# Kernel tuning notes

Measured on AMD Instinct MI355X. Metric: run time of the kernel, lower is better.

Reference implementation:

```python
import jax, jax.numpy as jnp
import numpy as np

B, MAXN, D, H, S = 64, 512, 512, 8, 32
DH = D // H          # per-head dim = 64
N = B * MAXN         # 32768 total nodes
E = 524288           # ~avg degree 16
EPS = 1e-5


def setup_inputs() -> dict:
    key = jax.random.key(0)
    ks = jax.random.split(key, 18)
    s = 0.05
    x_dense = jax.random.normal(ks[0], (B, MAXN, D), jnp.float32)
    x = jax.random.normal(ks[1], (N, D), jnp.float32)
    src = jax.random.randint(ks[2], (E,), 0, N)
    # destinations kept within the same graph as the source
    dst = (src // MAXN) * MAXN + jax.random.randint(ks[3], (E,), 0, MAXN)
    edge_index = jnp.stack([src, dst]).astype(jnp.int32)
    batch = (jnp.arange(N) // MAXN).astype(jnp.int32)  # sorted, 512 nodes/graph
    seed = jax.random.normal(ks[4], (S, 1, D), jnp.float32) * s
    # per-head GCN conv weights concatenated along output dim: [D, H*DH] == [D, D]
    Wk = jax.random.normal(ks[5], (D, D), jnp.float32) * s
    bk = jnp.zeros((D,), jnp.float32)
    Wv = jax.random.normal(ks[6], (D, D), jnp.float32) * s
    bv = jnp.zeros((D,), jnp.float32)
    q_proj_weight = jax.random.normal(ks[7], (D, D), jnp.float32) * s
    Wo = jax.random.normal(ks[8], (D, D), jnp.float32) * s
    bo = jnp.zeros((D,), jnp.float32)
    Wff = jax.random.normal(ks[9], (D, D), jnp.float32) * s
    bff = jnp.zeros((D,), jnp.float32)
    gamma_h = jnp.ones((D,), jnp.float32)
    beta_h = jnp.zeros((D,), jnp.float32)
    gamma_z = jnp.ones((D,), jnp.float32)
    beta_z = jnp.zeros((D,), jnp.float32)
    return dict(x_dense=x_dense, x=x, edge_index=edge_index, batch=batch,
                seed=seed, Wk=Wk, bk=bk, Wv=Wv, bv=bv,
                q_proj_weight=q_proj_weight, Wo=Wo, bo=bo, Wff=Wff, bff=bff,
                gamma_h=gamma_h, beta_h=beta_h, gamma_z=gamma_z, beta_z=beta_z)


def _gcn(x, W, b, src, dst):
    # PyG GCNConv with self-loops + symmetric norm; all H heads fused via W [D, H*DH]
    xw = x @ W                                   # [N, D]
    idx = jnp.arange(N)
    src_f = jnp.concatenate([src, idx])
    dst_f = jnp.concatenate([dst, idx])
    deg = jax.ops.segment_sum(jnp.ones_like(dst_f, dtype=x.dtype), dst_f, num_segments=N)
    dinv = jax.lax.rsqrt(deg)                    # deg >= 1 (self-loops)
    norm = dinv[src_f] * dinv[dst_f]             # [E+N]
    out = jax.ops.segment_sum(xw[src_f] * norm[:, None], dst_f, num_segments=N)
    return out + b


def _to_dense(feat, batch):
    # to_dense_batch for sorted batch vector; padded slots are zeros
    counts = jax.ops.segment_sum(jnp.ones((N,), jnp.int32), batch, num_segments=B)
    start = jnp.cumsum(counts) - counts
    pos = jnp.arange(N) - start[batch]
    return jnp.zeros((B, MAXN, feat.shape[-1]), feat.dtype).at[batch, pos].set(feat)


def _layernorm(x, g, b):
    m = jnp.mean(x, -1, keepdims=True)
    v = jnp.mean(jnp.square(x - m), -1, keepdims=True)
    return (x - m) * jax.lax.rsqrt(v + EPS) * g + b


def reference(x_dense, x, edge_index, batch, seed, Wk, bk, Wv, bv,
              q_proj_weight, Wo, bo, Wff, bff, gamma_h, beta_h, gamma_z, beta_z):
    src, dst = edge_index[0], edge_index[1]
    k_nodes = _gcn(x, Wk, bk, src, dst)          # [N, D] (H heads concat)
    v_nodes = _gcn(x, Wv, bv, src, dst)
    k_dense = _to_dense(k_nodes, batch)          # [B, MAXN, D]
    v_dense = _to_dense(v_nodes, batch)

    # query: seed [S,1,D] repeated over batch -> [S,B,D]; q projection (F.linear)
    query = jnp.broadcast_to(seed, (S, B, D))
    q = jnp.einsum('sbd,ed->sbe', query, q_proj_weight)
    scale = 1.0 / jnp.sqrt(jnp.float32(DH))
    qh = (q * scale).reshape(S, B, H, DH).transpose(1, 2, 0, 3)     # [B,H,S,DH]
    kh = k_dense.reshape(B, MAXN, H, DH).transpose(0, 2, 1, 3)      # [B,H,N,DH]
    vh = v_dense.reshape(B, MAXN, H, DH).transpose(0, 2, 1, 3)
    scores = jnp.einsum('bhsd,bhnd->bhsn', qh, kh)                  # [B,H,S,MAXN]
    attn = jax.nn.softmax(scores, axis=-1)                          # no padding mask (faithful)
    ctx = jnp.einsum('bhsn,bhnd->bhsd', attn, vh)                   # [B,H,S,DH]
    ctx = ctx.transpose(0, 2, 1, 3).reshape(B, S, D)                # heads concat
    attn_out = ctx @ Wo.T + bo                                      # [B,S,D]

    query_bse = jnp.broadcast_to(seed.transpose(1, 0, 2), (B, S, D))
    embed = _layernorm(query_bse + attn_out, gamma_h, beta_h)
    embed = _layernorm(embed + embed @ Wff.T + bff, gamma_z, beta_z)
    return embed
```

## Files before the change

### kernel.cpp

```cpp
#include <hip/hip_runtime.h>
#include <hip/hip_bf16.h>

#define BN   64
#define MAXN 512
#define DIM  512
#define NH   8
#define NS   32
#define NN   32768
#define NE   524288
#define MP   (2048 * 512)

typedef __hip_bfloat16 bf16;
using bf16x8 = __attribute__((ext_vector_type(8))) short;
using f32x4  = __attribute__((ext_vector_type(4))) float;

__device__ int   g_cnt[NN];
__device__ int   g_cur[NN];
__device__ int   g_off[NN + 1];
__device__ int   g_csr[NE];
__device__ float g_dinv[NN];
__device__ bf16  g_xb[NN * DIM];
__device__ bf16  g_agg[NN * DIM];
__device__ bf16  g_aggT[NN * DIM];
__device__ bf16  g_qf[256 * DIM];
__device__ bf16  g_wob[DIM * DIM];
__device__ bf16  g_wvb[DIM * DIM];
__device__ bf16  g_wvo[DIM * 8 * DIM];
__device__ float g_bvo[DIM];
__device__ bf16  g_wffT[DIM * DIM];
__device__ float g_q[NS * DIM];
__device__ bf16  g_sc[BN * 256 * MAXN];
__device__ bf16  g_cp[BN * NS * 8 * DIM];
__device__ float g_part[8 * MP];
__device__ float g_h1[BN * NS * DIM];
__device__ bf16  g_h1b[BN * NS * DIM];

__device__ inline float bf2f(unsigned short u) {
    union { unsigned int i; float f; } x; x.i = ((unsigned int)u) << 16; return x.f;
}

__device__ inline void gll16(const bf16* g, bf16* l) {
    __builtin_amdgcn_global_load_lds(
        (const __attribute__((address_space(1))) void*)g,
        (__attribute__((address_space(3))) void*)l, 16, 0, 0);
}

__global__ void k_zero() {
    int i = blockIdx.x * 256 + threadIdx.x;
    if (i < NN) { g_cnt[i] = 0; g_cur[i] = 0; }
}

__global__ void k_count(const int* __restrict__ dst) {
    int e = blockIdx.x * 256 + threadIdx.x;
    if (e < NE) atomicAdd(&g_cnt[dst[e]], 1);
}

__global__ void k_scan() {
    __shared__ int part[1024];
    int t = threadIdx.x;
    int base = t * 32;
    int loc[32]; int s = 0;
#pragma unroll
    for (int i = 0; i < 32; i++) { loc[i] = g_cnt[base + i]; s += loc[i]; }
    part[t] = s; __syncthreads();
    for (int o = 1; o < 1024; o <<= 1) {
        int v = (t >= o) ? part[t - o] : 0;
        __syncthreads();
        part[t] += v;
        __syncthreads();
    }
    int ex = (t == 0) ? 0 : part[t - 1];
#pragma unroll
    for (int i = 0; i < 32; i++) {
        g_off[base + i] = ex; ex += loc[i];
        g_dinv[base + i] = rsqrtf(1.0f + (float)loc[i]);
    }
    if (t == 1023) g_off[NN] = ex;
}

__global__ void k_fill(const int* __restrict__ src, const int* __restrict__ dst) {
    int e = blockIdx.x * 256 + threadIdx.x;
    if (e < NE) {
        int d = dst[e];
        int p = atomicAdd(&g_cur[d], 1);
        g_csr[g_off[d] + p] = src[e];
    }
}

__global__ __launch_bounds__(256) void k_xb(const float* __restrict__ x) {
    long i = (long)(blockIdx.x * 256 + threadIdx.x) * 8;
    int node = (int)(i >> 9);
    float w = g_dinv[node];
    float4 a = *(const float4*)(x + i);
    float4 b = *(const float4*)(x + i + 4);
    float v[8] = {a.x, a.y, a.z, a.w, b.x, b.y, b.z, b.w};
    bf16x8 o;
#pragma unroll
    for (int j = 0; j < 8; j++) { bf16 t = __float2bfloat16(v[j] * w); o[j] = *(short*)&t; }
    *(bf16x8*)(g_xb + i) = o;
}

__global__ __launch_bounds__(256) void k_gather() {
    int bid = blockIdx.x;
    int lb = (bid & 7) * 1024 + (bid >> 3);
    int wave = threadIdx.x >> 6, lane = threadIdx.x & 63;
    int node = lb * 4 + wave;

    bf16x8 sv = ((const bf16x8*)(g_xb + (long)node * DIM))[lane];
    float acc[8];
#pragma unroll
    for (int j = 0; j < 8; j++) acc[j] = bf2f((unsigned short)sv[j]);

    int e = g_off[node], e1 = g_off[node + 1];
    for (; e + 4 <= e1; e += 4) {
        int s0 = g_csr[e], s1 = g_csr[e + 1], s2 = g_csr[e + 2], s3 = g_csr[e + 3];
        bf16x8 r0 = ((const bf16x8*)(g_xb + (long)s0 * DIM))[lane];
        bf16x8 r1 = ((const bf16x8*)(g_xb + (long)s1 * DIM))[lane];
        bf16x8 r2 = ((const bf16x8*)(g_xb + (long)s2 * DIM))[lane];
        bf16x8 r3 = ((const bf16x8*)(g_xb + (long)s3 * DIM))[lane];
#pragma unroll
        for (int j = 0; j < 8; j++)
            acc[j] += (bf2f((unsigned short)r0[j]) + bf2f((unsigned short)r1[j]))
                    + (bf2f((unsigned short)r2[j]) + bf2f((unsigned short)r3[j]));
    }
    for (; e < e1; e++) {
        int s0 = g_csr[e];
        bf16x8 r0 = ((const bf16x8*)(g_xb + (long)s0 * DIM))[lane];
#pragma unroll
        for (int j = 0; j < 8; j++) acc[j] += bf2f((unsigned short)r0[j]);
    }
    float dd = g_dinv[node];
    bf16x8 o;
#pragma unroll
    for (int j = 0; j < 8; j++) { bf16 t = __float2bfloat16(acc[j] * dd); o[j] = *(short*)&t; }
    ((bf16x8*)(g_agg + (long)node * DIM))[lane] = o;
}

__global__ __launch_bounds__(256) void k_aggT() {
    __shared__ unsigned short L[64][72];
    int id = blockIdx.x;
    int b = id >> 6, t = id & 63;
    int n0 = (t & 7) * 64, d0 = (t >> 3) * 64;
    int tid = threadIdx.x;
    const unsigned short* src = (const unsigned short*)g_agg + ((long)b * 512 + n0) * 512 + d0;
#pragma unroll
    for (int p = 0; p < 2; p++) {
        int r = (tid >> 3) + 32 * p, c = (tid & 7) * 8;
        *(int4*)&L[r][c] = *(const int4*)(src + (long)r * 512 + c);
    }
    __syncthreads();
    unsigned short* dst = (unsigned short*)g_aggT + ((long)b * 512 + d0) * 512 + n0;
#pragma unroll
    for (int p = 0; p < 2; p++) {
        int dr = (tid >> 3) + 32 * p, c0 = (tid & 7) * 8;
        unsigned short tmp[8];
#pragma unroll
        for (int j = 0; j < 8; j++) tmp[j] = L[c0 + j][dr];
        *(int4*)(dst + (long)dr * 512 + c0) = *(int4*)tmp;
    }
}

__global__ void k_qproj(const float* __restrict__ seed, const float* __restrict__ Wq) {
    int i = blockIdx.x * 256 + threadIdx.x;
    int s = i >> 9, e = i & 511;
    const float* sr = seed + s * DIM;
    const float* wr = Wq + e * DIM;
    float a0 = 0.f, a1 = 0.f;
    for (int d = 0; d < DIM; d += 8) {
        float4 a = *(const float4*)(sr + d);
        float4 b = *(const float4*)(wr + d);
        float4 c = *(const float4*)(sr + d + 4);
        float4 w = *(const float4*)(wr + d + 4);
        a0 += a.x * b.x + a.y * b.y + a.z * b.z + a.w * b.w;
        a1 += c.x * w.x + c.y * w.y + c.z * w.z + c.w * w.w;
    }
    g_q[i] = (a0 + a1) * 0.125f;
}

__global__ __launch_bounds__(256) void k_cvt(const float* __restrict__ Wo,
                                             const float* __restrict__ Wv,
                                             const float* __restrict__ Wff) {
    long t = blockIdx.x * 256 + threadIdx.x;
    const float* src; bf16* dst; long off;
    if (t < 32768)      { src = Wo;  dst = g_wob;  off = t; }
    else if (t < 65536) { src = Wv;  dst = g_wvb;  off = t - 32768; }
    else                { src = Wff; dst = g_wffT; off = t - 65536; }
    long i = off * 8;
    float4 a = *(const float4*)(src + i);
    float4 b = *(const float4*)(src + i + 4);
    float v[8] = {a.x, a.y, a.z, a.w, b.x, b.y, b.z, b.w};
    bf16x8 o;
#pragma unroll
    for (int j = 0; j < 8; j++) { bf16 q = __float2bfloat16(v[j]); o[j] = *(short*)&q; }
    *(bf16x8*)(dst + i) = o;
}

__global__ __launch_bounds__(256) void k_qf(const float* __restrict__ Wk) {
    int i = blockIdx.x * 256 + threadIdx.x;
    int hs = i >> 9, d = i & 511;
    int h = hs >> 5, s = hs & 31;
    const float* qr = g_q + s * DIM + h * 64;
    const float* wr = Wk + d * DIM + h * 64;
    float a0 = 0.f, a1 = 0.f;
    for (int t2 = 0; t2 < 64; t2 += 8) {
        float4 a = *(const float4*)(qr + t2);
        float4 w = *(const float4*)(wr + t2);
        float4 c = *(const float4*)(qr + t2 + 4);
        float4 u = *(const float4*)(wr + t2 + 4);
        a0 += a.x * w.x + a.y * w.y + a.z * w.z + a.w * w.w;
        a1 += c.x * u.x + c.y * u.y + c.z * u.z + c.w * u.w;
    }
    g_qf[i] = __float2bfloat16(a0 + a1);
}

__global__ __launch_bounds__(256) void k_bvo(const float* __restrict__ bo,
                                             const float* __restrict__ bv,
                                             const float* __restrict__ Wo) {
    int e = blockIdx.x * 256 + threadIdx.x;
    const float* orow = Wo + (long)e * DIM;
    float a0 = 0.f, a1 = 0.f;
    for (int c = 0; c < DIM; c += 8) {
        float4 a = *(const float4*)(bv + c);
        float4 w = *(const float4*)(orow + c);
        float4 x = *(const float4*)(bv + c + 4);
        float4 u = *(const float4*)(orow + c + 4);
        a0 += a.x * w.x + a.y * w.y + a.z * w.z + a.w * w.w;
        a1 += x.x * u.x + x.y * u.y + x.z * u.z + x.w * u.w;
    }
    g_bvo[e] = bo[e] + a0 + a1;
}

__device__ __forceinline__ void gemm128(const bf16* __restrict__ A, long lda,
                                        const bf16* __restrict__ Bt, long ldb,
                                        long row0, long col0, int kbeg, int kend,
                                        bf16 (*As)[128 * 32], bf16 (*Bs)[128 * 32],
                                        f32x4 acc[4][4]) {
    int tid = threadIdx.x;
    int lane = tid & 63, wave = tid >> 6;
    int wr = wave >> 1, wc = wave & 1;
    int fr = lane & 15, fq = lane >> 4;
    int rchunk = (fq ^ ((fr >> 1) & 3)) * 8;
    int u0 = wave * 128 + lane;
    int sr0 = u0 >> 2, sc0 = ((u0 & 3) ^ ((sr0 >> 1) & 3)) * 8;
    int u1 = u0 + 64;
    int sr1 = u1 >> 2, sc1 = ((u1 & 3) ^ ((sr1 >> 1) & 3)) * 8;

    auto stage = [&](int buf, int kt) {
        gll16(A + (row0 + sr0) * lda + kt + sc0, As[buf] + u0 * 8);
        gll16(A + (row0 + sr1) * lda + kt + sc1, As[buf] + u1 * 8);
        gll16(Bt + (col0 + sr0) * ldb + kt + sc0, Bs[buf] + u0 * 8);
        gll16(Bt + (col0 + sr1) * ldb + kt + sc1, Bs[buf] + u1 * 8);
    };

    stage(0, kbeg);
    __syncthreads();
    for (int kt = kbeg; kt < kend; kt += 32) {
        int buf = ((kt - kbeg) >> 5) & 1;
        if (kt + 32 < kend) stage(buf ^ 1, kt + 32);
        bf16x8 af[4], bfv[4];
#pragma unroll
        for (int mi = 0; mi < 4; mi++)
            af[mi] = *(const bf16x8*)(As[buf] + (wr * 64 + mi * 16 + fr) * 32 + rchunk);
#pragma unroll
        for (int ni = 0; ni < 4; ni++)
            bfv[ni] = *(const bf16x8*)(Bs[buf] + (wc * 64 + ni * 16 + fr) * 32 + rchunk);
#pragma unroll
        for (int mi = 0; mi < 4; mi++)
#pragma unroll
            for (int ni = 0; ni < 4; ni++)
                acc[mi][ni] = __builtin_amdgcn_mfma_f32_16x16x32_bf16(af[mi], bfv[ni], acc[mi][ni], 0, 0, 0);
        __syncthreads();
    }
}

#define GEMM_PROLOGUE                                        \
    __shared__ bf16 As[2][128 * 32];                         \
    __shared__ bf16 Bs[2][128 * 32];                         \
    f32x4 acc[4][4];                                         \
    _Pragma("unroll")                                        \
    for (int i = 0; i < 4; i++)                              \
        _Pragma("unroll")                                    \
        for (int j = 0; j < 4; j++) acc[i][j] = (f32x4){0.f, 0.f, 0.f, 0.f}; \
    int lane = threadIdx.x & 63, wave = threadIdx.x >> 6;    \
    int wr = wave >> 1, wc = wave & 1;                       \
    int fr = lane & 15, fq = lane >> 4;

__global__ __launch_bounds__(256) void k_wvo() {
    GEMM_PROLOGUE
    int h = blockIdx.z;
    long row0 = (long)blockIdx.x * 128, col0 = (long)blockIdx.y * 128;
    gemm128(g_wob, DIM, g_wvb, DIM, row0, col0, h * 64, h * 64 + 64, As, Bs, acc);
#pragma unroll
    for (int mi = 0; mi < 4; mi++)
#pragma unroll
        for (int ni = 0; ni < 4; ni++) {
            long col = col0 + wc * 64 + ni * 16 + fr;
#pragma unroll
            for (int r = 0; r < 4; r++) {
                long row = row0 + wr * 64 + mi * 16 + fq * 4 + r;
                g_wvo[row * 4096 + h * 512 + col] = __float2bfloat16(acc[mi][ni][r]);
            }
        }
}

__global__ __launch_bounds__(256) void k_scores() {
    GEMM_PROLOGUE
    int b = blockIdx.z;
    long row0 = (long)blockIdx.x * 128, col0 = (long)blockIdx.y * 128;
    gemm128(g_qf, DIM, g_agg + (long)b * (MAXN * DIM), DIM, row0, col0, 0, DIM, As, Bs, acc);
    bf16* out = g_sc + (long)b * (256 * MAXN);
#pragma unroll
    for (int mi = 0; mi < 4; mi++)
#pragma unroll
        for (int ni = 0; ni < 4; ni++) {
            long col = col0 + wc * 64 + ni * 16 + fr;
#pragma unroll
            for (int r = 0; r < 4; r++) {
                long row = row0 + wr * 64 + mi * 16 + fq * 4 + r;
                out[row * MAXN + col] = __float2bfloat16(acc[mi][ni][r]);
            }
        }
}

__global__ __launch_bounds__(256) void k_soft() {
    int w = threadIdx.x >> 6, lane = threadIdx.x & 63;
    unsigned short* base = (unsigned short*)g_sc + ((long)blockIdx.x * 16 + w * 4) * MAXN;
#pragma unroll
    for (int r = 0; r < 4; r++) {
        unsigned short* row = base + (long)r * MAXN;
        float v[8]; float m = -1e30f;
#pragma unroll
        for (int k = 0; k < 8; k++) { v[k] = bf2f(row[lane + 64 * k]); m = fmaxf(m, v[k]); }
#pragma unroll
        for (int o = 32; o > 0; o >>= 1) m = fmaxf(m, __shfl_xor(m, o));
        float sum = 0.f;
#pragma unroll
        for (int k = 0; k < 8; k++) { v[k] = __expf(v[k] - m); sum += v[k]; }
#pragma unroll
        for (int o = 32; o > 0; o >>= 1) sum += __shfl_xor(sum, o);
        float inv = 1.0f / sum;
#pragma unroll
        for (int k = 0; k < 8; k++) {
            bf16 t = __float2bfloat16(v[k] * inv);
            row[lane + 64 * k] = *(unsigned short*)&t;
        }
    }
}

__global__ __launch_bounds__(256) void k_pvg() {
    GEMM_PROLOGUE
    int z = blockIdx.z, b = z >> 1, dh = z & 1;
    long row0 = (long)blockIdx.x * 128, col0 = (long)blockIdx.y * 128;
    gemm128(g_sc + (long)b * (256 * MAXN), MAXN,
            g_aggT + (long)b * (DIM * MAXN) + (long)dh * (256 * MAXN), MAXN,
            row0, col0, 0, MAXN, As, Bs, acc);
#pragma unroll
    for (int mi = 0; mi < 4; mi++)
#pragma unroll
        for (int ni = 0; ni < 4; ni++) {
            long col = col0 + wc * 64 + ni * 16 + fr;
#pragma unroll
            for (int r = 0; r < 4; r++) {
                long row = row0 + wr * 64 + mi * 16 + fq * 4 + r;
                g_cp[((long)b * NS + (row & 31)) * 4096 + (row >> 5) * 512 + dh * 256 + col] =
                    __float2bfloat16(acc[mi][ni][r]);
            }
        }
}

__global__ __launch_bounds__(256) void k_vo() {
    GEMM_PROLOGUE
    int z = blockIdx.z;
    long row0 = (long)blockIdx.x * 128, col0 = (long)blockIdx.y * 128;
    gemm128(g_cp, 4096, g_wvo, 4096, row0, col0, z * 512, z * 512 + 512, As, Bs, acc);
    float* out = g_part + (long)z * MP;
#pragma unroll
    for (int mi = 0; mi < 4; mi++)
#pragma unroll
        for (int ni = 0; ni < 4; ni++) {
            long col = col0 + wc * 64 + ni * 16 + fr;
#pragma unroll
            for (int r = 0; r < 4; r++) {
                long row = row0 + wr * 64 + mi * 16 + fq * 4 + r;
                out[row * DIM + col] = acc[mi][ni][r];
            }
        }
}

__global__ __launch_bounds__(256) void k_ffn() {
    GEMM_PROLOGUE
    int z = blockIdx.z;
    long row0 = (long)blockIdx.x * 128, col0 = (long)blockIdx.y * 128;
    gemm128(g_h1b, DIM, g_wffT, DIM, row0, col0, z * 128, z * 128 + 128, As, Bs, acc);
    float* out = g_part + (long)z * MP;
#pragma unroll
    for (int mi = 0; mi < 4; mi++)
#pragma unroll
        for (int ni = 0; ni < 4; ni++) {
            long col = col0 + wc * 64 + ni * 16 + fr;
#pragma unroll
            for (int r = 0; r < 4; r++) {
                long row = row0 + wr * 64 + mi * 16 + fq * 4 + r;
                out[row * DIM + col] = acc[mi][ni][r];
            }
        }
}

__device__ inline float blockReduceSum(float v, float* red, int tid) {
#pragma unroll
    for (int o = 32; o > 0; o >>= 1) v += __shfl_xor(v, o);
    __syncthreads();
    if ((tid & 63) == 0) red[tid >> 6] = v;
    __syncthreads();
    return red[0] + red[1] + red[2] + red[3];
}

__global__ __launch_bounds__(256) void k_ln1(const float* __restrict__ seed,
                                             const float* __restrict__ gamma,
                                             const float* __restrict__ beta) {
    __shared__ float red[4];
    int r = blockIdx.x, t = threadIdx.x;
    int s = r & 31;
    long base = (long)r * DIM;
    float v0 = seed[s * DIM + t] + g_bvo[t];
    float v1 = seed[s * DIM + 256 + t] + g_bvo[256 + t];
#pragma unroll
    for (int z = 0; z < 8; z++) {
        v0 += g_part[(long)z * MP + base + t];
        v1 += g_part[(long)z * MP + base + 256 + t];
    }
    float mean = blockReduceSum(v0 + v1, red, t) * (1.0f / DIM);
    float d0 = v0 - mean, d1 = v1 - mean;
    float var = blockReduceSum(d0 * d0 + d1 * d1, red, t) * (1.0f / DIM);
    float ri = rsqrtf(var + 1e-5f);
    float o0 = d0 * ri * gamma[t] + beta[t];
    float o1 = d1 * ri * gamma[256 + t] + beta[256 + t];
    g_h1[base + t] = o0; g_h1[base + 256 + t] = o1;
    g_h1b[base + t] = __float2bfloat16(o0);
    g_h1b[base + 256 + t] = __float2bfloat16(o1);
}

__global__ __launch_bounds__(256) void k_ln2(const float* __restrict__ gamma,
                                             const float* __restrict__ beta,
                                             const float* __restrict__ bff,
                                             float* __restrict__ out) {
    __shared__ float red[4];
    int r = blockIdx.x, t = threadIdx.x;
    long base = (long)r * DIM;
    float v0 = g_h1[base + t] + bff[t];
    float v1 = g_h1[base + 256 + t] + bff[256 + t];
#pragma unroll
    for (int z = 0; z < 4; z++) {
        v0 += g_part[(long)z * MP + base + t];
        v1 += g_part[(long)z * MP + base + 256 + t];
    }
    float mean = blockReduceSum(v0 + v1, red, t) * (1.0f / DIM);
    float d0 = v0 - mean, d1 = v1 - mean;
    float var = blockReduceSum(d0 * d0 + d1 * d1, red, t) * (1.0f / DIM);
    float ri = rsqrtf(var + 1e-5f);
    out[base + t] = d0 * ri * gamma[t] + beta[t];
    out[base + 256 + t] = d1 * ri * gamma[256 + t] + beta[256 + t];
}

extern "C" void kernel_launch(void* const* d_in, const int* in_sizes, int n_in,
                              void* d_out, int out_size, void* d_ws, size_t ws_size,
                              hipStream_t stream) {
    (void)in_sizes; (void)n_in; (void)out_size; (void)d_ws; (void)ws_size;
    const float* x    = (const float*)d_in[1];
    const int*   ei   = (const int*)d_in[2];
    const int*   esrc = ei;
    const int*   edst = ei + NE;
    const float* seed = (const float*)d_in[4];
    const float* Wk   = (const float*)d_in[5];
    const float* Wv   = (const float*)d_in[7];
    const float* bv   = (const float*)d_in[8];
    const float* Wq   = (const float*)d_in[9];
    const float* Wo   = (const float*)d_in[10];
    const float* bo   = (const float*)d_in[11];
    const float* Wff  = (const float*)d_in[12];
    const float* bff  = (const float*)d_in[13];
    const float* gh   = (const float*)d_in[14];
    const float* bh   = (const float*)d_in[15];
    const float* gz   = (const float*)d_in[16];
    const float* bz   = (const float*)d_in[17];
    float* out = (float*)d_out;

    k_zero <<<NN / 256, 256, 0, stream>>>();
    k_count<<<NE / 256, 256, 0, stream>>>(edst);
    k_scan <<<1, 1024, 0, stream>>>();
    k_fill <<<NE / 256, 256, 0, stream>>>(esrc, edst);
    k_xb   <<<(NN * DIM) / (256 * 8), 256, 0, stream>>>(x);
    k_gather<<<NN / 4, 256, 0, stream>>>();
    k_aggT <<<BN * 64, 256, 0, stream>>>();
    k_qproj<<<(NS * DIM) / 256, 256, 0, stream>>>(seed, Wq);
    k_cvt  <<<384, 256, 0, stream>>>(Wo, Wv, Wff);
    k_qf   <<<512, 256, 0, stream>>>(Wk);
    k_wvo  <<<dim3(4, 4, 8), 256, 0, stream>>>();
    k_bvo  <<<2, 256, 0, stream>>>(bo, bv, Wo);

    k_scores<<<dim3(2, 4, BN), 256, 0, stream>>>();
    k_soft  <<<1024, 256, 0, stream>>>();
    k_pvg   <<<dim3(2, 2, BN * 2), 256, 0, stream>>>();

    k_vo <<<dim3(16, 4, 8), 256, 0, stream>>>();
    k_ln1<<<BN * NS, 256, 0, stream>>>(seed, gh, bh);
    k_ffn<<<dim3(16, 4, 4), 256, 0, stream>>>();
    k_ln2<<<BN * NS, 256, 0, stream>>>(gz, bz, bff, out);
}
```

Baseline: 270.5 us.

## Fuse scores, softmax and PV into one attention kernel; merge prep kernels

Replaces the separate scores GEMM, softmax and PV GEMM with a single per-(graph, head) kernel. It computes scores into registers, does the softmax in-block, stores the probabilities in shared memory and multiplies by the transposed aggregate, so the bf16 score buffer round-trip through global memory goes away. The small prep kernels (q projection, weight conversion, qf, Wvo and bias folding) are merged into two launches to cut launch overhead. The Vo split-K drops from 8 to 4, which halves the partial-sum traffic read by the first layernorm. The fused kernel uses a large amount of shared memory and only 512 blocks, so occupancy may be low.

```diff
diff --git a/kernel.cpp b/kernel.cpp
--- a/kernel.cpp
+++ b/kernel.cpp
@@ -29,9 +29,8 @@
 __device__ float g_bvo[DIM];
 __device__ bf16  g_wffT[DIM * DIM];
 __device__ float g_q[NS * DIM];
-__device__ bf16  g_sc[BN * 256 * MAXN];
 __device__ bf16  g_cp[BN * NS * 8 * DIM];
-__device__ float g_part[8 * MP];
+__device__ float g_part[4 * MP];
 __device__ float g_h1[BN * NS * DIM];
 __device__ bf16  g_h1b[BN * NS * DIM];
 
@@ -160,74 +159,57 @@
     }
 }
 
-__global__ void k_qproj(const float* __restrict__ seed, const float* __restrict__ Wq) {
-    int i = blockIdx.x * 256 + threadIdx.x;
-    int s = i >> 9, e = i & 511;
-    const float* sr = seed + s * DIM;
-    const float* wr = Wq + e * DIM;
-    float a0 = 0.f, a1 = 0.f;
-    for (int d = 0; d < DIM; d += 8) {
-        float4 a = *(const float4*)(sr + d);
-        float4 b = *(const float4*)(wr + d);
-        float4 c = *(const float4*)(sr + d + 4);
-        float4 w = *(const float4*)(wr + d + 4);
-        a0 += a.x * b.x + a.y * b.y + a.z * b.z + a.w * b.w;
-        a1 += c.x * w.x + c.y * w.y + c.z * w.z + c.w * w.w;
-    }
-    g_q[i] = (a0 + a1) * 0.125f;
-}
-
-__global__ __launch_bounds__(256) void k_cvt(const float* __restrict__ Wo,
-                                             const float* __restrict__ Wv,
-                                             const float* __restrict__ Wff) {
-    long t = blockIdx.x * 256 + threadIdx.x;
-    const float* src; bf16* dst; long off;
-    if (t < 32768)      { src = Wo;  dst = g_wob;  off = t; }
-    else if (t < 65536) { src = Wv;  dst = g_wvb;  off = t - 32768; }
-    else                { src = Wff; dst = g_wffT; off = t - 65536; }
-    long i = off * 8;
-    float4 a = *(const float4*)(src + i);
-    float4 b = *(const float4*)(src + i + 4);
-    float v[8] = {a.x, a.y, a.z, a.w, b.x, b.y, b.z, b.w};
-    bf16x8 o;
-#pragma unroll
-    for (int j = 0; j < 8; j++) { bf16 q = __float2bfloat16(v[j]); o[j] = *(short*)&q; }
-    *(bf16x8*)(dst + i) = o;
-}
-
-__global__ __launch_bounds__(256) void k_qf(const float* __restrict__ Wk) {
-    int i = blockIdx.x * 256 + threadIdx.x;
-    int hs = i >> 9, d = i & 511;
-    int h = hs >> 5, s = hs & 31;
-    const float* qr = g_q + s * DIM + h * 64;
-    const float* wr = Wk + d * DIM + h * 64;
-    float a0 = 0.f, a1 = 0.f;
-    for (int t2 = 0; t2 < 64; t2 += 8) {
-        float4 a = *(const float4*)(qr + t2);
-        float4 w = *(const float4*)(wr + t2);
-        float4 c = *(const float4*)(qr + t2 + 4);
-        float4 u = *(const float4*)(wr + t2 + 4);
-        a0 += a.x * w.x + a.y * w.y + a.z * w.z + a.w * w.w;
-        a1 += c.x * u.x + c.y * u.y + c.z * u.z + c.w * u.w;
-    }
-    g_qf[i] = __float2bfloat16(a0 + a1);
-}
-
-__global__ __launch_bounds__(256) void k_bvo(const float* __restrict__ bo,
-                                             const float* __restrict__ bv,
-                                             const float* __restrict__ Wo) {
-    int e = blockIdx.x * 256 + threadIdx.x;
-    const float* orow = Wo + (long)e * DIM;
-    float a0 = 0.f, a1 = 0.f;
-    for (int c = 0; c < DIM; c += 8) {
-        float4 a = *(const float4*)(bv + c);
-        float4 w = *(const float4*)(orow + c);
-        float4 x = *(const float4*)(bv + c + 4);
-        float4 u = *(const float4*)(orow + c + 4);
-        a0 += a.x * w.x + a.y * w.y + a.z * w.z + a.w * w.w;
-        a1 += x.x * u.x + x.y * u.y + x.z * u.z + x.w * u.w;
-    }
-    g_bvo[e] = bo[e] + a0 + a1;
+__global__ __launch_bounds__(256) void k_prep(const float* __restrict__ seed,
+                                              const float* __restrict__ Wq,
+                                              const float* __restrict__ Wo,
+                                              const float* __restrict__ Wv,
+                                              const float* __restrict__ Wff,
+                                              const float* __restrict__ bo,
+                                              const float* __restrict__ bv) {
+    int blk = blockIdx.x;
+    if (blk < 64) {
+        int i = blk * 256 + threadIdx.x;
+        int s = i >> 9, e = i & 511;
+        const float* sr = seed + s * DIM;
+        const float* wr = Wq + e * DIM;
+        float a0 = 0.f, a1 = 0.f;
+        for (int d = 0; d < DIM; d += 8) {
+            float4 a = *(const float4*)(sr + d);
+            float4 b = *(const float4*)(wr + d);
+            float4 c = *(const float4*)(sr + d + 4);
+            float4 w = *(const float4*)(wr + d + 4);
+            a0 += a.x * b.x + a.y * b.y + a.z * b.z + a.w * b.w;
+            a1 += c.x * w.x + c.y * w.y + c.z * w.z + c.w * w.w;
+        }
+        g_q[i] = (a0 + a1) * 0.125f;
+    } else if (blk < 448) {
+        long t = (long)(blk - 64) * 256 + threadIdx.x;
+        const float* src; bf16* dst; long off;
+        if (t < 32768)      { src = Wo;  dst = g_wob;  off = t; }
+        else if (t < 65536) { src = Wv;  dst = g_wvb;  off = t - 32768; }
+        else                { src = Wff; dst = g_wffT; off = t - 65536; }
+        long i = off * 8;
+        float4 a = *(const float4*)(src + i);
+        float4 b = *(const float4*)(src + i + 4);
+        float v[8] = {a.x, a.y, a.z, a.w, b.x, b.y, b.z, b.w};
+        bf16x8 o;
+#pragma unroll
+        for (int j = 0; j < 8; j++) { bf16 q = __float2bfloat16(v[j]); o[j] = *(short*)&q; }
+        *(bf16x8*)(dst + i) = o;
+    } else {
+        int e = (blk - 448) * 256 + threadIdx.x;
+        const float* orow = Wo + (long)e * DIM;
+        float a0 = 0.f, a1 = 0.f;
+        for (int c = 0; c < DIM; c += 8) {
+            float4 a = *(const float4*)(bv + c);
+            float4 w = *(const float4*)(orow + c);
+            float4 x = *(const float4*)(bv + c + 4);
+            float4 u = *(const float4*)(orow + c + 4);
+            a0 += a.x * w.x + a.y * w.y + a.z * w.z + a.w * w.w;
+            a1 += x.x * u.x + x.y * u.y + x.z * u.z + x.w * u.w;
+        }
+        g_bvo[e] = bo[e] + a0 + a1;
+    }
 }
 
 __device__ __forceinline__ void gemm128(const bf16* __restrict__ A, long lda,
@@ -273,6 +255,202 @@
     }
 }
 
+__global__ __launch_bounds__(256) void k_qfwvo(const float* __restrict__ Wk) {
+    __shared__ bf16 As[2][128 * 32];
+    __shared__ bf16 Bs[2][128 * 32];
+    int blk = blockIdx.x;
+    if (blk < 512) {
+        int i = blk * 256 + threadIdx.x;
+        int hs = i >> 9, d = i & 511;
+        int h = hs >> 5, s = hs & 31;
+        const float* qr = g_q + s * DIM + h * 64;
+        const float* wr = Wk + d * DIM + h * 64;
+        float a0 = 0.f, a1 = 0.f;
+        for (int t2 = 0; t2 < 64; t2 += 8) {
+            float4 a = *(const float4*)(qr + t2);
+            float4 w = *(const float4*)(wr + t2);
+            float4 c = *(const float4*)(qr + t2 + 4);
+            float4 u = *(const float4*)(wr + t2 + 4);
+            a0 += a.x * w.x + a.y * w.y + a.z * w.z + a.w * w.w;
+            a1 += c.x * u.x + c.y * u.y + c.z * u.z + c.w * u.w;
+        }
+        g_qf[i] = __float2bfloat16(a0 + a1);
+    } else {
+        int wi = blk - 512;
+        int bx = wi & 3, by = (wi >> 2) & 3, h = wi >> 4;
+        f32x4 acc[4][4];
+#pragma unroll
+        for (int i = 0; i < 4; i++)
+#pragma unroll
+            for (int j = 0; j < 4; j++) acc[i][j] = (f32x4){0.f, 0.f, 0.f, 0.f};
+        int lane = threadIdx.x & 63;
+        int wr = (threadIdx.x >> 6) >> 1, wc = (threadIdx.x >> 6) & 1;
+        int fr = lane & 15, fq = lane >> 4;
+        long row0 = (long)bx * 128, col0 = (long)by * 128;
+        gemm128(g_wob, DIM, g_wvb, DIM, row0, col0, h * 64, h * 64 + 64, As, Bs, acc);
+#pragma unroll
+        for (int mi = 0; mi < 4; mi++)
+#pragma unroll
+            for (int ni = 0; ni < 4; ni++) {
+                long col = col0 + wc * 64 + ni * 16 + fr;
+#pragma unroll
+                for (int r = 0; r < 4; r++) {
+                    long row = row0 + wr * 64 + mi * 16 + fq * 4 + r;
+                    g_wvo[row * 4096 + h * 512 + col] = __float2bfloat16(acc[mi][ni][r]);
+                }
+            }
+    }
+}
+
+__global__ __launch_bounds__(256) void k_attn2() {
+    __shared__ bf16 Bs[2][512 * 32];
+    __shared__ bf16 Asq[2][32 * 32];
+    __shared__ bf16 P[32 * 512];
+    __shared__ float redm[4][32];
+    __shared__ float reds[4][32];
+    int z = blockIdx.x;
+    int b = z & 63, h = z >> 6;
+    int tid = threadIdx.x, lane = tid & 63, w = tid >> 6;
+    int fr = lane & 15, fq = lane >> 4;
+    int rchunk = (fq ^ ((fr >> 1) & 3)) * 8;
+
+    const bf16* Aq = g_qf + (long)(h * 32) * DIM;
+    const bf16* Bn = g_agg + (long)b * ((long)MAXN * DIM);
+    const bf16* Bd = g_aggT + (long)b * ((long)DIM * MAXN);
+
+    int brow[8], bcol[8];
+#pragma unroll
+    for (int c = 0; c < 8; c++) {
+        int u = tid + 256 * c;
+        brow[c] = u >> 2;
+        bcol[c] = ((u & 3) ^ ((brow[c] >> 1) & 3)) * 8;
+    }
+    int arow = tid >> 2;
+    int acol = ((tid & 3) ^ ((arow >> 1) & 3)) * 8;
+
+    f32x4 acc[2][8];
+#pragma unroll
+    for (int i = 0; i < 2; i++)
+#pragma unroll
+        for (int j = 0; j < 8; j++) acc[i][j] = (f32x4){0.f, 0.f, 0.f, 0.f};
+
+    if (tid < 128) gll16(Aq + (long)arow * DIM + acol, Asq[0] + tid * 8);
+#pragma unroll
+    for (int c = 0; c < 8; c++)
+        gll16(Bn + (long)brow[c] * DIM + bcol[c], Bs[0] + (tid + 256 * c) * 8);
+    __syncthreads();
+    for (int kt = 0; kt < 512; kt += 32) {
+        int buf = (kt >> 5) & 1;
+        if (kt + 32 < 512) {
+            if (tid < 128) gll16(Aq + (long)arow * DIM + kt + 32 + acol, Asq[buf ^ 1] + tid * 8);
+#pragma unroll
+            for (int c = 0; c < 8; c++)
+                gll16(Bn + (long)brow[c] * DIM + kt + 32 + bcol[c], Bs[buf ^ 1] + (tid + 256 * c) * 8);
+        } else {
+#pragma unroll
+            for (int c = 0; c < 8; c++)
+                gll16(Bd + (long)brow[c] * MAXN + bcol[c], Bs[0] + (tid + 256 * c) * 8);
+        }
+        bf16x8 af[2], bv8[8];
+#pragma unroll
+        for (int mi = 0; mi < 2; mi++)
+            af[mi] = *(const bf16x8*)(Asq[buf] + (mi * 16 + fr) * 32 + rchunk);
+#pragma unroll
+        for (int nf = 0; nf < 8; nf++)
+            bv8[nf] = *(const bf16x8*)(Bs[buf] + (w * 128 + nf * 16 + fr) * 32 + rchunk);
+#pragma unroll
+        for (int mi = 0; mi < 2; mi++)
+#pragma unroll
+            for (int nf = 0; nf < 8; nf++)
+                acc[mi][nf] = __builtin_amdgcn_mfma_f32_16x16x32_bf16(af[mi], bv8[nf], acc[mi][nf], 0, 0, 0);
+        __syncthreads();
+    }
+
+#pragma unroll
+    for (int mi = 0; mi < 2; mi++)
+#pragma unroll
+        for (int r = 0; r < 4; r++) {
+            float m = acc[mi][0][r];
+#pragma unroll
+            for (int nf = 1; nf < 8; nf++) m = fmaxf(m, acc[mi][nf][r]);
+#pragma unroll
+            for (int o = 1; o < 16; o <<= 1) m = fmaxf(m, __shfl_xor(m, o));
+            if (fr == 0) redm[w][mi * 16 + fq * 4 + r] = m;
+        }
+    __syncthreads();
+#pragma unroll
+    for (int mi = 0; mi < 2; mi++)
+#pragma unroll
+        for (int r = 0; r < 4; r++) {
+            int row = mi * 16 + fq * 4 + r;
+            float M = fmaxf(fmaxf(redm[0][row], redm[1][row]), fmaxf(redm[2][row], redm[3][row]));
+            float s = 0.f;
+#pragma unroll
+            for (int nf = 0; nf < 8; nf++) {
+                float e = __expf(acc[mi][nf][r] - M);
+                acc[mi][nf][r] = e; s += e;
+            }
+#pragma unroll
+            for (int o = 1; o < 16; o <<= 1) s += __shfl_xor(s, o);
+            if (fr == 0) reds[w][row] = s;
+        }
+    __syncthreads();
+#pragma unroll
+    for (int mi = 0; mi < 2; mi++)
+#pragma unroll
+        for (int r = 0; r < 4; r++) {
+            int row = mi * 16 + fq * 4 + r;
+            float iv = 1.0f / (reds[0][row] + reds[1][row] + reds[2][row] + reds[3][row]);
+#pragma unroll
+            for (int nf = 0; nf < 8; nf++) {
+                int col = w * 128 + nf * 16 + fr;
+                int ch = (col >> 3) ^ (row & 7);
+                P[row * 512 + ch * 8 + (col & 7)] = __float2bfloat16(acc[mi][nf][r] * iv);
+            }
+        }
+    __syncthreads();
+
+#pragma unroll
+    for (int i = 0; i < 2; i++)
+#pragma unroll
+        for (int j = 0; j < 8; j++) acc[i][j] = (f32x4){0.f, 0.f, 0.f, 0.f};
+    for (int kt = 0; kt < 512; kt += 32) {
+        int buf = (kt >> 5) & 1;
+        if (kt + 32 < 512) {
+#pragma unroll
+            for (int c = 0; c < 8; c++)
+                gll16(Bd + (long)brow[c] * MAXN + kt + 32 + bcol[c], Bs[buf ^ 1] + (tid + 256 * c) * 8);
+        }
+        bf16x8 af2[2], bv8[8];
+#pragma unroll
+        for (int mi = 0; mi < 2; mi++) {
+            int row = mi * 16 + fr;
+            int ch = ((kt >> 3) + fq) ^ (row & 7);
+            af2[mi] = *(const bf16x8*)(P + row * 512 + ch * 8);
+        }
+#pragma unroll
+        for (int nf = 0; nf < 8; nf++)
+            bv8[nf] = *(const bf16x8*)(Bs[buf] + (w * 128 + nf * 16 + fr) * 32 + rchunk);
+#pragma unroll
+        for (int mi = 0; mi < 2; mi++)
+#pragma unroll
+            for (int nf = 0; nf < 8; nf++)
+                acc[mi][nf] = __builtin_amdgcn_mfma_f32_16x16x32_bf16(af2[mi], bv8[nf], acc[mi][nf], 0, 0, 0);
+        __syncthreads();
+    }
+#pragma unroll
+    for (int mi = 0; mi < 2; mi++)
+#pragma unroll
+        for (int nf = 0; nf < 8; nf++) {
+            int d = w * 128 + nf * 16 + fr;
+#pragma unroll
+            for (int r = 0; r < 4; r++) {
+                int s = mi * 16 + fq * 4 + r;
+                g_cp[((long)b * NS + s) * 4096 + h * 512 + d] = __float2bfloat16(acc[mi][nf][r]);
+            }
+        }
+}
+
 #define GEMM_PROLOGUE                                        \
     __shared__ bf16 As[2][128 * 32];                         \
     __shared__ bf16 Bs[2][128 * 32];                         \
@@ -285,94 +463,11 @@
     int wr = wave >> 1, wc = wave & 1;                       \
     int fr = lane & 15, fq = lane >> 4;
 
-__global__ __launch_bounds__(256) void k_wvo() {
-    GEMM_PROLOGUE
-    int h = blockIdx.z;
-    long row0 = (long)blockIdx.x * 128, col0 = (long)blockIdx.y * 128;
-    gemm128(g_wob, DIM, g_wvb, DIM, row0, col0, h * 64, h * 64 + 64, As, Bs, acc);
-#pragma unroll
-    for (int mi = 0; mi < 4; mi++)
-#pragma unroll
-        for (int ni = 0; ni < 4; ni++) {
-            long col = col0 + wc * 64 + ni * 16 + fr;
-#pragma unroll
-            for (int r = 0; r < 4; r++) {
-                long row = row0 + wr * 64 + mi * 16 + fq * 4 + r;
-                g_wvo[row * 4096 + h * 512 + col] = __float2bfloat16(acc[mi][ni][r]);
-            }
-        }
-}
-
-__global__ __launch_bounds__(256) void k_scores() {
-    GEMM_PROLOGUE
-    int b = blockIdx.z;
-    long row0 = (long)blockIdx.x * 128, col0 = (long)blockIdx.y * 128;
-    gemm128(g_qf, DIM, g_agg + (long)b * (MAXN * DIM), DIM, row0, col0, 0, DIM, As, Bs, acc);
-    bf16* out = g_sc + (long)b * (256 * MAXN);
-#pragma unroll
-    for (int mi = 0; mi < 4; mi++)
-#pragma unroll
-        for (int ni = 0; ni < 4; ni++) {
-            long col = col0 + wc * 64 + ni * 16 + fr;
-#pragma unroll
-            for (int r = 0; r < 4; r++) {
-                long row = row0 + wr * 64 + mi * 16 + fq * 4 + r;
-                out[row * MAXN + col] = __float2bfloat16(acc[mi][ni][r]);
-            }
-        }
-}
-
-__global__ __launch_bounds__(256) void k_soft() {
-    int w = threadIdx.x >> 6, lane = threadIdx.x & 63;
-    unsigned short* base = (unsigned short*)g_sc + ((long)blockIdx.x * 16 + w * 4) * MAXN;
-#pragma unroll
-    for (int r = 0; r < 4; r++) {
-        unsigned short* row = base + (long)r * MAXN;
-        float v[8]; float m = -1e30f;
-#pragma unroll
-        for (int k = 0; k < 8; k++) { v[k] = bf2f(row[lane + 64 * k]); m = fmaxf(m, v[k]); }
-#pragma unroll
-        for (int o = 32; o > 0; o >>= 1) m = fmaxf(m, __shfl_xor(m, o));
-        float sum = 0.f;
-#pragma unroll
-        for (int k = 0; k < 8; k++) { v[k] = __expf(v[k] - m); sum += v[k]; }
-#pragma unroll
-        for (int o = 32; o > 0; o >>= 1) sum += __shfl_xor(sum, o);
-        float inv = 1.0f / sum;
-#pragma unroll
-        for (int k = 0; k < 8; k++) {
-            bf16 t = __float2bfloat16(v[k] * inv);
-            row[lane + 64 * k] = *(unsigned short*)&t;
-        }
-    }
-}
-
-__global__ __launch_bounds__(256) void k_pvg() {
-    GEMM_PROLOGUE
-    int z = blockIdx.z, b = z >> 1, dh = z & 1;
-    long row0 = (long)blockIdx.x * 128, col0 = (long)blockIdx.y * 128;
-    gemm128(g_sc + (long)b * (256 * MAXN), MAXN,
-            g_aggT + (long)b * (DIM * MAXN) + (long)dh * (256 * MAXN), MAXN,
-            row0, col0, 0, MAXN, As, Bs, acc);
-#pragma unroll
-    for (int mi = 0; mi < 4; mi++)
-#pragma unroll
-        for (int ni = 0; ni < 4; ni++) {
-            long col = col0 + wc * 64 + ni * 16 + fr;
-#pragma unroll
-            for (int r = 0; r < 4; r++) {
-                long row = row0 + wr * 64 + mi * 16 + fq * 4 + r;
-                g_cp[((long)b * NS + (row & 31)) * 4096 + (row >> 5) * 512 + dh * 256 + col] =
-                    __float2bfloat16(acc[mi][ni][r]);
-            }
-        }
-}
-
 __global__ __launch_bounds__(256) void k_vo() {
     GEMM_PROLOGUE
     int z = blockIdx.z;
     long row0 = (long)blockIdx.x * 128, col0 = (long)blockIdx.y * 128;
-    gemm128(g_cp, 4096, g_wvo, 4096, row0, col0, z * 512, z * 512 + 512, As, Bs, acc);
+    gemm128(g_cp, 4096, g_wvo, 4096, row0, col0, z * 1024, z * 1024 + 1024, As, Bs, acc);
     float* out = g_part + (long)z * MP;
 #pragma unroll
     for (int mi = 0; mi < 4; mi++)
@@ -425,7 +520,7 @@
     float v0 = seed[s * DIM + t] + g_bvo[t];
     float v1 = seed[s * DIM + 256 + t] + g_bvo[256 + t];
 #pragma unroll
-    for (int z = 0; z < 8; z++) {
+    for (int z = 0; z < 4; z++) {
         v0 += g_part[(long)z * MP + base + t];
         v1 += g_part[(long)z * MP + base + 256 + t];
     }
@@ -492,17 +587,12 @@
     k_xb   <<<(NN * DIM) / (256 * 8), 256, 0, stream>>>(x);
     k_gather<<<NN / 4, 256, 0, stream>>>();
     k_aggT <<<BN * 64, 256, 0, stream>>>();
-    k_qproj<<<(NS * DIM) / 256, 256, 0, stream>>>(seed, Wq);
-    k_cvt  <<<384, 256, 0, stream>>>(Wo, Wv, Wff);
-    k_qf   <<<512, 256, 0, stream>>>(Wk);
-    k_wvo  <<<dim3(4, 4, 8), 256, 0, stream>>>();
-    k_bvo  <<<2, 256, 0, stream>>>(bo, bv, Wo);
-
-    k_scores<<<dim3(2, 4, BN), 256, 0, stream>>>();
-    k_soft  <<<1024, 256, 0, stream>>>();
-    k_pvg   <<<dim3(2, 2, BN * 2), 256, 0, stream>>>();
-
-    k_vo <<<dim3(16, 4, 8), 256, 0, stream>>>();
+    k_prep <<<450, 256, 0, stream>>>(seed, Wq, Wo, Wv, Wff, bo, bv);
+    k_qfwvo<<<640, 256, 0, stream>>>(Wk);
+
+    k_attn2<<<512, 256, 0, stream>>>();
+
+    k_vo <<<dim3(16, 4, 4), 256, 0, stream>>>();
     k_ln1<<<BN * NS, 256, 0, stream>>>(seed, gh, bh);
     k_ffn<<<dim3(16, 4, 4), 256, 0, stream>>>();
     k_ln2<<<BN * NS, 256, 0, stream>>>(gz, bz, bff, out);
```

Result: slower. 279.4 us (+3.3%).
